# Performance work log

Measured on AMD Instinct MI355X. Metric: run time of the kernel, lower is better.

Reference implementation:

```python
import jax, jax.numpy as jnp
import numpy as np

B, S, D, H, DFF, L = 32, 512, 512, 8, 2048, 3
DK = D // H
NEG = -1e32


def _ln(x, g, b):
    m = jnp.mean(x, axis=-1, keepdims=True)
    v = jnp.mean((x - m) ** 2, axis=-1, keepdims=True)
    return (x - m) / jnp.sqrt(v + 1e-5) * g + b


def _mha(query, key, value, mask, zero_pad, gam, Wk, bk, Wv, bv, Wo, bo):
    # kq_same: q and k both use k_linear
    q = (query @ Wk + bk).reshape(B, S, H, DK).transpose(0, 2, 1, 3)
    k = (key @ Wk + bk).reshape(B, S, H, DK).transpose(0, 2, 1, 3)
    v = (value @ Wv + bv).reshape(B, S, H, DK).transpose(0, 2, 1, 3)
    scores = jnp.einsum('bhid,bhjd->bhij', q, k) / jnp.sqrt(jnp.float32(DK))
    # distance-decay rescoring (no-grad in original)
    p = jax.nn.softmax(jnp.where(mask, scores, NEG), axis=-1) * mask
    distcum = jnp.cumsum(p, axis=-1)
    disttotal = jnp.sum(p, axis=-1, keepdims=True)
    idx = jnp.arange(S)
    pos = jnp.abs(idx[None, :] - idx[:, None]).astype(jnp.float32)  # [S,S]
    dist = jax.lax.stop_gradient(
        jnp.sqrt(jnp.clip((disttotal - distcum) * pos[None, None], 0.0, None)))
    gamma = -jax.nn.softplus(gam)[None, :, None, None]  # [1,H,1,1]
    total_effect = jnp.clip(jnp.exp(dist * gamma), 1e-5, 1e5)
    scores = jnp.where(mask, scores * total_effect, NEG)
    scores = jax.nn.softmax(scores, axis=-1)
    if zero_pad:
        scores = scores * (idx[:, None] > 0)[None, None, :, :].astype(scores.dtype) * 0 + \
                 scores * (idx > 0).astype(scores.dtype)[None, None, :, None]
    out = jnp.einsum('bhij,bhjd->bhid', scores, v)
    out = out.transpose(0, 2, 1, 3).reshape(B, S, D)
    return out @ Wo + bo


def _layer(i, mask, zero_pad, query, key, values, apply_pos,
           Wk, bk, Wv, bv, Wo, bo, gammas, ln1_g, ln1_b, W1, b1, W2, b2, ln2_g, ln2_b):
    a = _mha(query, key, values, mask, zero_pad, gammas[i],
             Wk[i], bk[i], Wv[i], bv[i], Wo[i], bo[i])
    x = _ln(query + a, ln1_g[i], ln1_b[i])
    if apply_pos:
        f = jax.nn.relu(x @ W1[i] + b1[i]) @ W2[i] + b2[i]
        x = _ln(x + f, ln2_g[i], ln2_b[i])
    return x


def setup_inputs() -> dict:
    key = jax.random.key(0)
    ks = jax.random.split(key, 12)
    sc = 0.02
    inp = {
        'q_embed_data': jax.random.normal(ks[0], (B, S, D), jnp.float32),
        'qa_embed_data': jax.random.normal(ks[1], (B, S, D), jnp.float32),
        'Wk': jax.random.normal(ks[2], (L, D, D), jnp.float32) * sc,
        'bk': jnp.zeros((L, D), jnp.float32),
        'Wv': jax.random.normal(ks[3], (L, D, D), jnp.float32) * sc,
        'bv': jnp.zeros((L, D), jnp.float32),
        'Wo': jax.random.normal(ks[4], (L, D, D), jnp.float32) * sc,
        'bo': jnp.zeros((L, D), jnp.float32),
        'gammas': jax.random.normal(ks[5], (L, H), jnp.float32) * 0.5,
        'ln1_g': jnp.ones((L, D), jnp.float32),
        'ln1_b': jnp.zeros((L, D), jnp.float32),
        'W1': jax.random.normal(ks[6], (L, D, DFF), jnp.float32) * sc,
        'b1': jnp.zeros((L, DFF), jnp.float32),
        'W2': jax.random.normal(ks[7], (L, DFF, D), jnp.float32) * sc,
        'b2': jnp.zeros((L, D), jnp.float32),
        'ln2_g': jnp.ones((L, D), jnp.float32),
        'ln2_b': jnp.zeros((L, D), jnp.float32),
    }
    return inp


def reference(q_embed_data, qa_embed_data, Wk, bk, Wv, bv, Wo, bo, gammas,
              ln1_g, ln1_b, W1, b1, W2, b2, ln2_g, ln2_b):
    P = (Wk, bk, Wv, bv, Wo, bo, gammas, ln1_g, ln1_b, W1, b1, W2, b2, ln2_g, ln2_b)
    mask1 = jnp.tril(jnp.ones((S, S), bool), 0)[None, None]   # peek current+past
    mask0 = jnp.tril(jnp.ones((S, S), bool), -1)[None, None]  # peek only past
    y = qa_embed_data
    x = q_embed_data
    # blocks_1 (n_blocks=1): mask=1, self-attn, apply_pos
    y = _layer(0, mask1, False, y, y, y, True, *P)
    # blocks_2 (2 layers): first mask=1 no FFN, second mask=0 zero_pad cross-attn to y
    x = _layer(1, mask1, False, x, x, x, False, *P)
    x = _layer(2, mask0, True, x, x, y, True, *P)
    return x
```

## Files before the change

### kernel.cpp

```cpp
#include <hip/hip_runtime.h>

#define BB   32
#define SS   512
#define DDIM 512
#define HH   8
#define DFFN 2048
#define MR   (BB*SS)

typedef unsigned int   u32;
typedef unsigned short u16;
typedef unsigned char  u8;
typedef __attribute__((ext_vector_type(8))) short bf16x8;
typedef __attribute__((ext_vector_type(4))) float f32x4;

__device__ __forceinline__ u32 packbf2(float x, float y) {
  u32 ux = __float_as_uint(x), uy = __float_as_uint(y);
  u32 hx = (ux + 0x7FFFu + ((ux >> 16) & 1u)) >> 16;
  u32 hy = (uy + 0x7FFFu + ((uy >> 16) & 1u)) >> 16;
  return hx | (hy << 16);
}
__device__ __forceinline__ u16 pack1bf(float x) {
  u32 u = __float_as_uint(x);
  return (u16)((u + 0x7FFFu + ((u >> 16) & 1u)) >> 16);
}

__device__ __forceinline__ float redsum2(float v) {
  v += __shfl_xor(v, 16, 64);
  v += __shfl_xor(v, 32, 64);
  return v;
}

__device__ __forceinline__ float expc(float x) { return __expf(fminf(x, 80.f)); }

__global__ __launch_bounds__(256) void pack_flat(const float* __restrict__ in,
                                                 u16* __restrict__ out) {
  size_t i = ((size_t)blockIdx.x * 256 + threadIdx.x) * 8;
  float4 a = *(const float4*)(in + i);
  float4 b = *(const float4*)(in + i + 4);
  uint4 o;
  o.x = packbf2(a.x, a.y); o.y = packbf2(a.z, a.w);
  o.z = packbf2(b.x, b.y); o.w = packbf2(b.z, b.w);
  *(uint4*)(out + i) = o;
}

__global__ __launch_bounds__(256) void pack_w_t(const float* __restrict__ in,
                                                u16* __restrict__ out, int K, int N) {
  __shared__ float tile[64][65];
  const int t  = threadIdx.x;
  const int n0 = blockIdx.x * 64, k0 = blockIdx.y * 64;
  in  += (size_t)blockIdx.z * K * N;
  out += (size_t)blockIdx.z * N * K;
  #pragma unroll
  for (int it = 0; it < 4; ++it) {
    int idx = it * 256 + t;
    int kk = idx >> 4, n4 = idx & 15;
    float4 v = *(const float4*)(in + (size_t)(k0 + kk) * N + n0 + n4 * 4);
    tile[kk][n4*4+0] = v.x; tile[kk][n4*4+1] = v.y;
    tile[kk][n4*4+2] = v.z; tile[kk][n4*4+3] = v.w;
  }
  __syncthreads();
  #pragma unroll
  for (int it = 0; it < 4; ++it) {
    int idx = it * 256 + t;
    int nn = idx >> 4, g = idx & 15;
    uint2 o;
    o.x = packbf2(tile[g*4+0][nn], tile[g*4+1][nn]);
    o.y = packbf2(tile[g*4+2][nn], tile[g*4+3][nn]);
    *(uint2*)(out + (size_t)(n0 + nn) * K + k0 + g * 4) = o;
  }
}

__global__ __launch_bounds__(512, 2) void gemm8(
    const u16* __restrict__ Aa, const u16* __restrict__ Ab, int lda,
    const u16* __restrict__ Ba, const u16* __restrict__ Bb, int ldb,
    const float* __restrict__ biasa, const float* __restrict__ biasb,
    float* __restrict__ outFa, float* __restrict__ outFb,
    u16* __restrict__ outBa, u16* __restrict__ outBb,
    int ldc, int Kz, int relu, float sca, float scb)
{
  __shared__ __align__(16) u8 lds[131072];

  const int z = blockIdx.z;
  const u16* A    = z ? Ab : Aa;
  const u16* Bt   = z ? Bb : Ba;
  const float* bias = z ? biasb : biasa;
  float* outF = z ? outFb : outFa;
  u16*   outB = z ? outBb : outBa;
  const float sc = z ? scb : sca;

  const int nwg  = gridDim.x * gridDim.y;
  const int orig = blockIdx.y * gridDim.x + blockIdx.x;
  const int q8   = nwg >> 3, r8 = nwg & 7;
  const int xcd  = orig & 7, idx8 = orig >> 3;
  const int wg   = (xcd < r8 ? xcd * (q8 + 1) : r8 * (q8 + 1) + (xcd - r8) * q8) + idx8;
  const int bx   = wg % gridDim.x, by = wg / gridDim.x;
  const int row0 = by * 256, col0 = bx * 256;

  const int t    = threadIdx.x;
  const int lane = t & 63, wid = t >> 6;
  const int wm   = wid >> 2, wn = wid & 3;
  const int rl   = lane & 15, kg = lane >> 4;

  const int NT = Kz >> 6;

  f32x4 acc[8][4] = {};

  auto stageA = [&](int buf, int h, int kt) {
    #pragma unroll
    for (int l = 0; l < 2; ++l) {
      int s  = (l * 512 + t) >> 3;
      int kb = ((lane & 7) * 16) ^ ((s & 7) << 4);
      int row = row0 + ((s >> 6) * 128) + h * 64 + (s & 63);
      const u8* src = (const u8*)A + (size_t)row * lda * 2 + (size_t)kt * 128 + kb;
      u8* dst = lds + buf * 65536 + h * 16384 + (l * 512 + wid * 64) * 16;
      __builtin_amdgcn_global_load_lds(
          (const __attribute__((address_space(1))) u32*)src,
          (__attribute__((address_space(3))) u32*)dst, 16, 0, 0);
    }
  };
  auto stageB = [&](int buf, int h, int kt) {
    #pragma unroll
    for (int l = 0; l < 2; ++l) {
      int s  = (l * 512 + t) >> 3;
      int kb = ((lane & 7) * 16) ^ ((s & 7) << 4);
      int col = col0 + ((s >> 5) * 64) + h * 32 + (s & 31);
      const u8* src = (const u8*)Bt + (size_t)col * ldb * 2 + (size_t)kt * 128 + kb;
      u8* dst = lds + buf * 65536 + 32768 + h * 16384 + (l * 512 + wid * 64) * 16;
      __builtin_amdgcn_global_load_lds(
          (const __attribute__((address_space(1))) u32*)src,
          (__attribute__((address_space(3))) u32*)dst, 16, 0, 0);
    }
  };

  auto rdA = [&](int buf, int mh, int m, int ks) -> bf16x8 {
    int s = wm * 64 + m * 16 + rl;
    int off = buf * 65536 + mh * 16384 + s * 128 + (((ks * 32 + kg * 8) * 2) ^ ((s & 7) << 4));
    return *(const bf16x8*)(lds + off);
  };
  auto rdB = [&](int buf, int nh, int n, int ks) -> bf16x8 {
    int s = wn * 32 + n * 16 + rl;
    int off = buf * 65536 + 32768 + nh * 16384 + s * 128 + (((ks * 32 + kg * 8) * 2) ^ ((s & 7) << 4));
    return *(const bf16x8*)(lds + off);
  };

#define GBAR asm volatile("s_barrier" ::: "memory")
#define VMW4 asm volatile("s_waitcnt vmcnt(4)" ::: "memory")

#define PHASE(BUF, MH, NH, STAGECODE, DOVM) do {                               \
    bf16x8 af_[4][2], bf_[2][2];                                               \
    _Pragma("unroll") for (int m_ = 0; m_ < 4; ++m_)                           \
      _Pragma("unroll") for (int k_ = 0; k_ < 2; ++k_)                         \
        af_[m_][k_] = rdA(BUF, MH, m_, k_);                                    \
    _Pragma("unroll") for (int n_ = 0; n_ < 2; ++n_)                           \
      _Pragma("unroll") for (int k_ = 0; k_ < 2; ++k_)                         \
        bf_[n_][k_] = rdB(BUF, NH, n_, k_);                                    \
    STAGECODE;                                                                 \
    if (DOVM) VMW4;                                                            \
    GBAR;                                                                      \
    __builtin_amdgcn_s_setprio(1);                                             \
    _Pragma("unroll") for (int m_ = 0; m_ < 4; ++m_)                           \
      _Pragma("unroll") for (int n_ = 0; n_ < 2; ++n_) {                       \
        acc[(MH)*4+m_][(NH)*2+n_] = __builtin_amdgcn_mfma_f32_16x16x32_bf16(   \
            af_[m_][0], bf_[n_][0], acc[(MH)*4+m_][(NH)*2+n_], 0, 0, 0);       \
        acc[(MH)*4+m_][(NH)*2+n_] = __builtin_amdgcn_mfma_f32_16x16x32_bf16(   \
            af_[m_][1], bf_[n_][1], acc[(MH)*4+m_][(NH)*2+n_], 0, 0, 0);       \
      }                                                                        \
    __builtin_amdgcn_s_setprio(0);                                             \
    GBAR;                                                                      \
  } while (0)

  stageA(0, 0, 0); stageB(0, 0, 0); stageA(0, 1, 0); stageB(0, 1, 0);
  stageA(1, 0, 1); stageB(1, 0, 1);
  VMW4; GBAR;

  for (int i = 0; i < (NT >> 1); ++i) {
    const int T1 = 2 * i + 1;
    int T2 = 2 * i + 2; if (T2 >= NT) T2 -= NT;
    int T3 = 2 * i + 3; if (T3 >= NT) T3 -= NT;
    PHASE(0, 0, 0, stageA(1, 1, T1), 0);
    PHASE(0, 0, 1, stageB(1, 1, T1), 0);
    PHASE(0, 1, 0, stageA(0, 0, T2), 0);
    PHASE(0, 1, 1, stageB(0, 0, T2), 1);
    PHASE(1, 0, 0, stageA(0, 1, T2), 0);
    PHASE(1, 0, 1, stageB(0, 1, T2), 0);
    PHASE(1, 1, 0, stageA(1, 0, T3), 0);
    PHASE(1, 1, 1, stageB(1, 0, T3), 1);
  }
#undef PHASE
#undef GBAR
#undef VMW4

  #pragma unroll
  for (int M = 0; M < 8; ++M) {
    #pragma unroll
    for (int N2 = 0; N2 < 4; ++N2) {
      const int col = col0 + wn * 64 + N2 * 16 + rl;
      const float bs = bias ? bias[col] : 0.f;
      #pragma unroll
      for (int q = 0; q < 4; ++q) {
        const int row = row0 + wm * 128 + M * 16 + kg * 4 + q;
        float v = (acc[M][N2][q] + bs) * sc;
        if (relu) v = fmaxf(v, 0.f);
        if (outF) outF[(size_t)row * ldc + col] = v;
        if (outB) outB[(size_t)row * ldc + col] = pack1bf(v);
      }
    }
  }
}

__global__ __attribute__((amdgpu_flat_work_group_size(512, 512)))
           __attribute__((amdgpu_waves_per_eu(1, 2)))
void attn_mfma(
    const u16* __restrict__ qk, const u16* __restrict__ vbuf,
    const float* __restrict__ gam, u16* __restrict__ out,
    int mask_excl, int zero_pad)
{
  __shared__ __align__(16) u8 kSb[65536];
  __shared__ __align__(16) u8 vTb[65536];
  __shared__ __align__(16) u8 pChb[8192];

  const int t    = threadIdx.x;
  const int lane = t & 63, wid = t >> 6;
  const int ql   = lane & 15, g = lane >> 4;
  const int bh   = blockIdx.x, b = bh >> 3, h = bh & 7;
  const size_t base = (size_t)b * SS * DDIM + (size_t)h * 64;

  float gv = gam[h];
  float sp = (gv > 0.f) ? (gv + log1pf(__expf(-gv))) : log1pf(__expf(gv));
  const float gamma = -sp;

  for (int it = 0; it < 8; ++it) {
    int idx = it * 512 + t;
    int j = idx >> 3, u = idx & 7;
    uint4 w = *(const uint4*)(qk + base + (size_t)j * DDIM + u * 8);
    *(uint4*)(kSb + ((j * 128 + u * 16) ^ ((j & 7) << 4))) = w;
  }
  for (int it = 0; it < 8; ++it) {
    int idx = it * 512 + t;
    int j = idx >> 3, u = idx & 7;
    union { uint4 v4; u16 s[8]; } uu;
    uu.v4 = *(const uint4*)(vbuf + base + (size_t)j * DDIM + u * 8);
    #pragma unroll
    for (int dd = 0; dd < 8; ++dd) {
      int d = u * 8 + dd;
      *(u16*)(vTb + d * 1024 + ((2 * j) ^ ((dd ^ u) << 4))) = uu.s[dd];
    }
  }
  __syncthreads();

  bool vm[4];
  #pragma unroll
  for (int rg = 0; rg < 4; ++rg) {
    int kl = 4 * g + rg;
    vm[rg] = mask_excl ? (kl < ql) : (kl <= ql);
  }

  u8* pB = pChb + wid * 1024;
  const int swp = (ql & 7) << 4;

  int vbase[4], vsw[4];
  #pragma unroll
  for (int n = 0; n < 4; ++n) {
    int d = n * 16 + ql;
    vbase[n] = d * 1024;
    vsw[n]   = ((d & 7) ^ ((d >> 3) & 7)) << 4;
  }

  #pragma unroll
  for (int ri = 0; ri < 4; ++ri) {
    int r0_ = (ri == 0) ? wid : (ri == 1) ? (15 - wid) : (ri == 2) ? (16 + wid) : (31 - wid);
    const int rs = __builtin_amdgcn_readfirstlane(r0_);
    const int i0 = rs * 16;

    const int qrow = i0 + ql;
    const int qsw  = (qrow & 7) << 4;
    bf16x8 qf0 = *(const bf16x8*)(kSb + ((qrow * 128      + g * 16) ^ qsw));
    bf16x8 qf1 = *(const bf16x8*)(kSb + ((qrow * 128 + 64 + g * 16) ^ qsw));

    float S1l = 0.f;
    #pragma unroll
    for (int kt = 0; kt < 32; ++kt) {
      if (kt <= rs) {
        const bool dg = (kt == rs);
        const int krow = kt * 16 + ql;
        const int ksw  = (krow & 7) << 4;
        bf16x8 ka0 = *(const bf16x8*)(kSb + ((krow * 128      + g * 16) ^ ksw));
        bf16x8 ka1 = *(const bf16x8*)(kSb + ((krow * 128 + 64 + g * 16) ^ ksw));
        f32x4 dv = {};
        dv = __builtin_amdgcn_mfma_f32_16x16x32_bf16(ka0, qf0, dv, 0, 0, 0);
        dv = __builtin_amdgcn_mfma_f32_16x16x32_bf16(ka1, qf1, dv, 0, 0, 0);
        float e0 = (!dg || vm[0]) ? expc(dv[0]) : 0.f;
        float e1 = (!dg || vm[1]) ? expc(dv[1]) : 0.f;
        float e2 = (!dg || vm[2]) ? expc(dv[2]) : 0.f;
        float e3 = (!dg || vm[3]) ? expc(dv[3]) : 0.f;
        S1l += (e0 + e1) + (e2 + e3);
      }
    }
    const float S1   = redsum2(S1l);
    const float inv1 = (S1 > 0.f) ? (1.f / S1) : 0.f;

    f32x4 oacc[4] = {};
    float cbase = 0.f, S2l = 0.f;
    const float qlf = (float)(i0 + ql);

    auto subkt = [&](int kt, bool dg, u32& wA, u32& wB) {
      const int krow = kt * 16 + ql;
      const int ksw  = (krow & 7) << 4;
      bf16x8 ka0 = *(const bf16x8*)(kSb + ((krow * 128      + g * 16) ^ ksw));
      bf16x8 ka1 = *(const bf16x8*)(kSb + ((krow * 128 + 64 + g * 16) ^ ksw));
      f32x4 dv = {};
      dv = __builtin_amdgcn_mfma_f32_16x16x32_bf16(ka0, qf0, dv, 0, 0, 0);
      dv = __builtin_amdgcn_mfma_f32_16x16x32_bf16(ka1, qf1, dv, 0, 0, 0);
      const bool v0 = !dg || vm[0], v1 = !dg || vm[1];
      const bool v2 = !dg || vm[2], v3 = !dg || vm[3];
      float e0 = v0 ? expc(dv[0]) : 0.f;
      float e1 = v1 ? expc(dv[1]) : 0.f;
      float e2 = v2 ? expc(dv[2]) : 0.f;
      float e3 = v3 ? expc(dv[3]) : 0.f;
      float p0 = e0, p1 = p0 + e1, p2 = p1 + e2, p3 = p2 + e3;
      float a16 = __shfl_up(p3, 16, 64);
      float a32 = __shfl_up(p3, 32, 64);
      float a48 = __shfl_up(p3, 48, 64);
      float gp = (g >= 1 ? a16 : 0.f) + (g >= 2 ? a32 : 0.f) + (g >= 3 ? a48 : 0.f);
      float tt = __shfl(gp + p3, ql + 48, 64);
      const float pbase = cbase + gp;
      const float pf = qlf - (float)(kt * 16 + 4 * g);
      float ipr[4] = {p0, p1, p2, p3};
      bool  vv[4]  = {v0, v1, v2, v3};
      float sv[4]  = {dv[0], dv[1], dv[2], dv[3]};
      float q2[4];
      #pragma unroll
      for (int rg = 0; rg < 4; ++rg) {
        float rem  = fmaxf((S1 - (pbase + ipr[rg])) * inv1, 0.f);
        float pos  = pf - (float)rg;
        float dist = sqrtf(fmaxf(rem * pos, 0.f));
        float eff  = fmaxf(__expf(gamma * dist), 1e-5f);
        float ee   = vv[rg] ? expc(sv[rg] * eff) : 0.f;
        q2[rg] = ee;
        S2l += ee;
      }
      wA = packbf2(q2[0], q2[1]);
      wB = packbf2(q2[2], q2[3]);
      cbase += tt;
    };

    #pragma unroll
    for (int c = 0; c < 16; ++c) {
      if (2 * c <= rs) {
        u32 w0 = 0, w1 = 0, w2 = 0, w3 = 0;
        subkt(2 * c, (2 * c == rs), w0, w1);
        if (2 * c + 1 <= rs) subkt(2 * c + 1, (2 * c + 1 == rs), w2, w3);
        *(u32*)(pB + ((ql * 64 +      8 * g    ) ^ swp)) = w0;
        *(u32*)(pB + ((ql * 64 +      8 * g + 4) ^ swp)) = w1;
        *(u32*)(pB + ((ql * 64 + 32 + 8 * g    ) ^ swp)) = w2;
        *(u32*)(pB + ((ql * 64 + 32 + 8 * g + 4) ^ swp)) = w3;
        bf16x8 pa = *(const bf16x8*)(pB + ((ql * 64 + 16 * g) ^ swp));
        #pragma unroll
        for (int n = 0; n < 4; ++n) {
          bf16x8 vb = *(const bf16x8*)(vTb + vbase[n] + ((64 * c + 16 * g) ^ vsw[n]));
          oacc[n] = __builtin_amdgcn_mfma_f32_16x16x32_bf16(pa, vb, oacc[n], 0, 0, 0);
        }
      }
    }

    const float S2   = redsum2(S2l);
    const float inv2 = 1.f / fmaxf(S2, 1e-30f);
    float i2[4];
    #pragma unroll
    for (int rg = 0; rg < 4; ++rg) i2[rg] = __shfl(inv2, 4 * g + rg, 64);

    #pragma unroll
    for (int n = 0; n < 4; ++n) {
      #pragma unroll
      for (int rg = 0; rg < 4; ++rg) {
        const int qo = i0 + 4 * g + rg;
        float val = oacc[n][rg] * i2[rg];
        if (zero_pad && qo == 0) val = 0.f;
        out[base + (size_t)qo * DDIM + n * 16 + ql] = pack1bf(val);
      }
    }
  }
}

__global__ __launch_bounds__(256) void ln_kernel(
    const u16* __restrict__ a, const float* __restrict__ bsrc,
    const float* __restrict__ csrc,
    const float* __restrict__ g, const float* __restrict__ be,
    float* __restrict__ outF, u16* __restrict__ outB)
{
  const int lane = threadIdx.x & 63, w = threadIdx.x >> 6;
  const size_t row = (size_t)blockIdx.x * 4 + w;
  const size_t off8 = row * DDIM + lane * 8;

  uint4 ab = *(const uint4*)(a + off8);
  const u16* ap = (const u16*)&ab;
  float v[8];
  #pragma unroll
  for (int k = 0; k < 8; ++k) v[k] = __uint_as_float(((u32)ap[k]) << 16);

  float4 b0 = *(const float4*)(bsrc + off8);
  float4 b1 = *(const float4*)(bsrc + off8 + 4);
  v[0] += b0.x; v[1] += b0.y; v[2] += b0.z; v[3] += b0.w;
  v[4] += b1.x; v[5] += b1.y; v[6] += b1.z; v[7] += b1.w;
  if (csrc) {
    float4 c0 = *(const float4*)(csrc + off8);
    float4 c1 = *(const float4*)(csrc + off8 + 4);
    v[0] += c0.x; v[1] += c0.y; v[2] += c0.z; v[3] += c0.w;
    v[4] += c1.x; v[5] += c1.y; v[6] += c1.z; v[7] += c1.w;
  }

  float sum = 0.f;
  #pragma unroll
  for (int k = 0; k < 8; ++k) sum += v[k];
  #pragma unroll
  for (int off = 32; off > 0; off >>= 1) sum += __shfl_xor(sum, off, 64);
  const float mean = sum * (1.f / 512.f);
  float var = 0.f;
  #pragma unroll
  for (int k = 0; k < 8; ++k) { float dd = v[k] - mean; var = fmaf(dd, dd, var); }
  #pragma unroll
  for (int off = 32; off > 0; off >>= 1) var += __shfl_xor(var, off, 64);
  var *= (1.f / 512.f);
  const float inv = rsqrtf(var + 1e-5f);

  float4 g0 = *(const float4*)(g + lane * 8);
  float4 g1 = *(const float4*)(g + lane * 8 + 4);
  float4 e0 = *(const float4*)(be + lane * 8);
  float4 e1 = *(const float4*)(be + lane * 8 + 4);
  float gv[8] = {g0.x, g0.y, g0.z, g0.w, g1.x, g1.y, g1.z, g1.w};
  float ev[8] = {e0.x, e0.y, e0.z, e0.w, e1.x, e1.y, e1.z, e1.w};
  float o[8];
  #pragma unroll
  for (int k = 0; k < 8; ++k) o[k] = (v[k] - mean) * inv * gv[k] + ev[k];

  if (outF) {
    float4 f0 = {o[0], o[1], o[2], o[3]};
    float4 f1 = {o[4], o[5], o[6], o[7]};
    *(float4*)(outF + off8)     = f0;
    *(float4*)(outF + off8 + 4) = f1;
  }
  if (outB) {
    uint4 p;
    p.x = packbf2(o[0], o[1]); p.y = packbf2(o[2], o[3]);
    p.z = packbf2(o[4], o[5]); p.w = packbf2(o[6], o[7]);
    *(uint4*)(outB + off8) = p;
  }
}

extern "C" void kernel_launch(void* const* d_in, const int* in_sizes, int n_in,
                              void* d_out, int out_size, void* d_ws, size_t ws_size,
                              hipStream_t stream) {
  const float* qe  = (const float*)d_in[0];
  const float* qa  = (const float*)d_in[1];
  const float* Wk  = (const float*)d_in[2];
  const float* bk  = (const float*)d_in[3];
  const float* Wv  = (const float*)d_in[4];
  const float* bv  = (const float*)d_in[5];
  const float* Wo  = (const float*)d_in[6];
  const float* bo  = (const float*)d_in[7];
  const float* gm  = (const float*)d_in[8];
  const float* l1g = (const float*)d_in[9];
  const float* l1b = (const float*)d_in[10];
  const float* W1  = (const float*)d_in[11];
  const float* b1  = (const float*)d_in[12];
  const float* W2  = (const float*)d_in[13];
  const float* b2  = (const float*)d_in[14];
  const float* l2g = (const float*)d_in[15];
  const float* l2b = (const float*)d_in[16];

  char* ws = (char*)d_ws;
  u16* WT = (u16*)ws;
  u16* A0 = (u16*)(ws + ((size_t)18  << 20));
  u16* A1 = (u16*)(ws + ((size_t)34  << 20));
  u16* A2 = (u16*)(ws + ((size_t)50  << 20));
  u16* A3 = (u16*)(ws + ((size_t)66  << 20));
  float* F0 = (float*)(ws + ((size_t)82  << 20));
  float* PW2 = (float*)(ws + ((size_t)114 << 20));
  u16* Amid = (u16*)(ws + ((size_t)146 << 20));
  float* PWo = (float*)Amid;

  u16* WkT = WT;
  u16* WvT = WT + (size_t)3 * 262144;
  u16* WoT = WT + (size_t)6 * 262144;
  u16* W1T = WT + (size_t)9 * 262144;
  u16* W2T = W1T + (size_t)3 * 1048576;

  pack_w_t<<<dim3(8, 8, 3),  256, 0, stream>>>(Wk, WkT, 512, 512);
  pack_w_t<<<dim3(8, 8, 3),  256, 0, stream>>>(Wv, WvT, 512, 512);
  pack_w_t<<<dim3(8, 8, 3),  256, 0, stream>>>(Wo, WoT, 512, 512);
  pack_w_t<<<dim3(32, 8, 3), 256, 0, stream>>>(W1, W1T, 512, 2048);
  pack_w_t<<<dim3(8, 32, 3), 256, 0, stream>>>(W2, W2T, 2048, 512);
  pack_flat<<<4096, 256, 0, stream>>>(qa, A0);
  pack_flat<<<4096, 256, 0, stream>>>(qe, A1);

  const float SQ = 0.35355339059327373f;

  auto g8 = [&](const u16* Aa, const u16* Ab, int lda,
                const u16* Ba, const u16* Bb, int ldb,
                const float* ba, const float* bb,
                float* oFa, float* oFb, u16* oBa, u16* oBb,
                int ldc, int M, int N, int Kz, int relu, int nz,
                float sca, float scb) {
    gemm8<<<dim3(N / 256, M / 256, nz), 512, 0, stream>>>(
        Aa, Ab, lda, Ba, Bb, ldb, ba, bb, oFa, oFb, oBa, oBb, ldc, Kz, relu,
        sca, scb);
  };

  auto layer = [&](int li, const u16* qbf, const u16* vbf,
                   int excl, int zp, int pos,
                   u16* x1B, u16* y2B, float* y2F) {
    const float* bk_l = bk + (size_t)li * DDIM;
    const float* bv_l = bv + (size_t)li * DDIM;
    const float* bo_l = bo + (size_t)li * DDIM;
    const float* gm_l = gm + (size_t)li * HH;
    const float* g1   = l1g + (size_t)li * DDIM;
    const float* be1  = l1b + (size_t)li * DDIM;
    const float* g2   = l2g + (size_t)li * DDIM;
    const float* be2  = l2b + (size_t)li * DDIM;
    const float* b1_l = b1 + (size_t)li * DFFN;
    const float* b2_l = b2 + (size_t)li * DDIM;
    const u16* WkT_l = WkT + (size_t)li * 262144;
    const u16* WvT_l = WvT + (size_t)li * 262144;
    const u16* WoT_l = WoT + (size_t)li * 262144;
    const u16* W1T_l = W1T + (size_t)li * 1048576;
    const u16* W2T_l = W2T + (size_t)li * 1048576;

    g8(qbf, vbf, 512, WkT_l, WvT_l, 512, bk_l, bv_l,
       nullptr, nullptr, A2, A3, 512, MR, 512, 512, 0, 2, SQ, 1.f);
    attn_mfma<<<BB * HH, 512, 0, stream>>>(A2, A3, gm_l, A3, excl, zp);
    g8(A3, A3 + 256, 512, WoT_l, WoT_l + 256, 512, bo_l, nullptr,
       F0, PWo, nullptr, nullptr, 512, MR, 512, 256, 0, 2, 1.f, 1.f);
    ln_kernel<<<MR / 4, 256, 0, stream>>>(qbf, F0, PWo, g1, be1, nullptr, x1B);
    if (pos) {
      g8(x1B, nullptr, 512, W1T_l, nullptr, 512, b1_l, nullptr,
         nullptr, nullptr, Amid, nullptr, 2048, MR, 2048, 512, 1, 1, 1.f, 1.f);
      g8(Amid, Amid + 1024, 2048, W2T_l, W2T_l + 1024, 2048, b2_l, nullptr,
         F0, PW2, nullptr, nullptr, 512, MR, 512, 1024, 0, 2, 1.f, 1.f);
      ln_kernel<<<MR / 4, 256, 0, stream>>>(x1B, F0, PW2, g2, be2, y2F, y2B);
    }
  };

  layer(0, A0, A0, 0, 0, 1, A2, A0, nullptr);
  layer(1, A1, A1, 0, 0, 0, A1, nullptr, nullptr);
  layer(2, A1, A0, 1, 1, 1, A1, nullptr, (float*)d_out);
}
```

Baseline: 700.0 us.

## Batch independent layer-0/1 attention stages into shared launches and use exp2

Layers 0 and 1 are independent up to their first LayerNorm, so their QKV projections, attention, output projections and LayerNorms now run together in single launches via job tables (4-way and 2-way grid z), raising occupancy for the smaller grids. Attention switches to base-2 exponentials with the log2e factor folded into the QK scale and gamma. The V transpose now writes packed 32-bit pairs. The GEMM loop gets a peeled tail that skips the wrap-around prefetch. Weight and input packing kernels are merged to cut launches, at the cost of more workspace buffers and a larger kernel parameter struct.

Result: faster. 656.5 us (-6.2%).

```diff
diff --git a/kernel.cpp b/kernel.cpp
--- a/kernel.cpp
+++ b/kernel.cpp
@@ -30,10 +30,27 @@
   return v;
 }
 
-__device__ __forceinline__ float expc(float x) { return __expf(fminf(x, 80.f)); }
-
-__global__ __launch_bounds__(256) void pack_flat(const float* __restrict__ in,
-                                                 u16* __restrict__ out) {
+#if __has_builtin(__builtin_amdgcn_exp2f)
+__device__ __forceinline__ float ex2c(float x) { return __builtin_amdgcn_exp2f(fminf(x, 110.f)); }
+__device__ __forceinline__ float ex2r(float x) { return __builtin_amdgcn_exp2f(x); }
+#else
+__device__ __forceinline__ float ex2c(float x) {
+  float r = fminf(x, 110.f);
+  asm("v_exp_f32 %0, %1" : "=v"(r) : "v"(r));
+  return r;
+}
+__device__ __forceinline__ float ex2r(float x) {
+  float r;
+  asm("v_exp_f32 %0, %1" : "=v"(r) : "v"(x));
+  return r;
+}
+#endif
+
+__global__ __launch_bounds__(256) void pack_flat2(
+    const float* __restrict__ in0, const float* __restrict__ in1,
+    u16* __restrict__ out0, u16* __restrict__ out1) {
+  const float* in = blockIdx.y ? in1 : in0;
+  u16* out = blockIdx.y ? out1 : out0;
   size_t i = ((size_t)blockIdx.x * 256 + threadIdx.x) * 8;
   float4 a = *(const float4*)(in + i);
   float4 b = *(const float4*)(in + i + 4);
@@ -43,13 +60,12 @@
   *(uint4*)(out + i) = o;
 }
 
-__global__ __launch_bounds__(256) void pack_w_t(const float* __restrict__ in,
-                                                u16* __restrict__ out, int K, int N) {
+__device__ __forceinline__ void wtp_body(const float* __restrict__ in,
+                                         u16* __restrict__ out, int K, int N,
+                                         int bx, int by) {
   __shared__ float tile[64][65];
   const int t  = threadIdx.x;
-  const int n0 = blockIdx.x * 64, k0 = blockIdx.y * 64;
-  in  += (size_t)blockIdx.z * K * N;
-  out += (size_t)blockIdx.z * N * K;
+  const int n0 = bx * 64, k0 = by * 64;
   #pragma unroll
   for (int it = 0; it < 4; ++it) {
     int idx = it * 256 + t;
@@ -69,24 +85,37 @@
     *(uint2*)(out + (size_t)(n0 + nn) * K + k0 + g * 4) = o;
   }
 }
+__global__ __launch_bounds__(256) void pack_w_t(const float* __restrict__ in,
+                                                u16* __restrict__ out, int K, int N) {
+  wtp_body(in + (size_t)blockIdx.z * K * N, out + (size_t)blockIdx.z * N * K,
+           K, N, blockIdx.x, blockIdx.y);
+}
+__global__ __launch_bounds__(256) void pack_w_sq(
+    const float* __restrict__ Wk, const float* __restrict__ Wv,
+    const float* __restrict__ Wo,
+    u16* __restrict__ WkT, u16* __restrict__ WvT, u16* __restrict__ WoT) {
+  const int z = blockIdx.z, which = z / 3, li = z % 3;
+  const float* in = (which == 0 ? Wk : which == 1 ? Wv : Wo) + (size_t)li * 262144;
+  u16* out = (which == 0 ? WkT : which == 1 ? WvT : WoT) + (size_t)li * 262144;
+  wtp_body(in, out, 512, 512, blockIdx.x, blockIdx.y);
+}
+
+struct GJob { const u16* A; const u16* Bt; const float* bias;
+              float* outF; u16* outB; float sc; };
+struct GJobs { GJob j[4]; };
 
 __global__ __launch_bounds__(512, 2) void gemm8(
-    const u16* __restrict__ Aa, const u16* __restrict__ Ab, int lda,
-    const u16* __restrict__ Ba, const u16* __restrict__ Bb, int ldb,
-    const float* __restrict__ biasa, const float* __restrict__ biasb,
-    float* __restrict__ outFa, float* __restrict__ outFb,
-    u16* __restrict__ outBa, u16* __restrict__ outBb,
-    int ldc, int Kz, int relu, float sca, float scb)
+    GJobs jobs, int lda, int ldb, int ldc, int Kz, int relu)
 {
   __shared__ __align__(16) u8 lds[131072];
 
-  const int z = blockIdx.z;
-  const u16* A    = z ? Ab : Aa;
-  const u16* Bt   = z ? Bb : Ba;
-  const float* bias = z ? biasb : biasa;
-  float* outF = z ? outFb : outFa;
-  u16*   outB = z ? outBb : outBa;
-  const float sc = z ? scb : sca;
+  const GJob J = jobs.j[blockIdx.z];
+  const u16* A    = J.A;
+  const u16* Bt   = J.Bt;
+  const float* bias = J.bias;
+  float* outF = J.outF;
+  u16*   outB = J.outB;
+  const float sc = J.sc;
 
   const int nwg  = gridDim.x * gridDim.y;
   const int orig = blockIdx.y * gridDim.x + blockIdx.x;
@@ -145,6 +174,7 @@
 
 #define GBAR asm volatile("s_barrier" ::: "memory")
 #define VMW4 asm volatile("s_waitcnt vmcnt(4)" ::: "memory")
+#define VMW0 asm volatile("s_waitcnt vmcnt(0)" ::: "memory")
 
 #define PHASE(BUF, MH, NH, STAGECODE, DOVM) do {                               \
     bf16x8 af_[4][2], bf_[2][2];                                               \
@@ -155,7 +185,8 @@
       _Pragma("unroll") for (int k_ = 0; k_ < 2; ++k_)                         \
         bf_[n_][k_] = rdB(BUF, NH, n_, k_);                                    \
     STAGECODE;                                                                 \
-    if (DOVM) VMW4;                                                            \
+    if (DOVM == 1) VMW4;                                                       \
+    if (DOVM == 2) VMW0;                                                       \
     GBAR;                                                                      \
     __builtin_amdgcn_s_setprio(1);                                             \
     _Pragma("unroll") for (int m_ = 0; m_ < 4; ++m_)                           \
@@ -173,10 +204,8 @@
   stageA(1, 0, 1); stageB(1, 0, 1);
   VMW4; GBAR;
 
-  for (int i = 0; i < (NT >> 1); ++i) {
-    const int T1 = 2 * i + 1;
-    int T2 = 2 * i + 2; if (T2 >= NT) T2 -= NT;
-    int T3 = 2 * i + 3; if (T3 >= NT) T3 -= NT;
+  for (int i = 0; i < (NT >> 1) - 1; ++i) {
+    const int T1 = 2 * i + 1, T2 = 2 * i + 2, T3 = 2 * i + 3;
     PHASE(0, 0, 0, stageA(1, 1, T1), 0);
     PHASE(0, 0, 1, stageB(1, 1, T1), 0);
     PHASE(0, 1, 0, stageA(0, 0, T2), 0);
@@ -186,9 +215,18 @@
     PHASE(1, 1, 0, stageA(1, 0, T3), 0);
     PHASE(1, 1, 1, stageB(1, 0, T3), 1);
   }
+  PHASE(0, 0, 0, stageA(1, 1, NT - 1), 0);
+  PHASE(0, 0, 1, stageB(1, 1, NT - 1), 0);
+  PHASE(0, 1, 0, ;, 0);
+  PHASE(0, 1, 1, ;, 2);
+  PHASE(1, 0, 0, ;, 0);
+  PHASE(1, 0, 1, ;, 0);
+  PHASE(1, 1, 0, ;, 0);
+  PHASE(1, 1, 1, ;, 0);
 #undef PHASE
 #undef GBAR
 #undef VMW4
+#undef VMW0
 
   #pragma unroll
   for (int M = 0; M < 8; ++M) {
@@ -211,9 +249,11 @@
 __global__ __attribute__((amdgpu_flat_work_group_size(512, 512)))
            __attribute__((amdgpu_waves_per_eu(1, 2)))
 void attn_mfma(
-    const u16* __restrict__ qk, const u16* __restrict__ vbuf,
-    const float* __restrict__ gam, u16* __restrict__ out,
-    int mask_excl, int zero_pad)
+    const u16* __restrict__ qkA, const u16* __restrict__ vbA,
+    const float* __restrict__ gmA, u16* __restrict__ outAp,
+    const u16* __restrict__ qkB, const u16* __restrict__ vbB,
+    const float* __restrict__ gmB, u16* __restrict__ outBp,
+    int nA, int mask_excl, int zero_pad)
 {
   __shared__ __align__(16) u8 kSb[65536];
   __shared__ __align__(16) u8 vTb[65536];
@@ -222,12 +262,19 @@
   const int t    = threadIdx.x;
   const int lane = t & 63, wid = t >> 6;
   const int ql   = lane & 15, g = lane >> 4;
-  const int bh   = blockIdx.x, b = bh >> 3, h = bh & 7;
+  const int bid  = blockIdx.x;
+  const int sel  = bid >= nA;
+  const u16* qk    = sel ? qkB : qkA;
+  const u16* vbuf  = sel ? vbB : vbA;
+  const float* gam = sel ? gmB : gmA;
+  u16* out         = sel ? outBp : outAp;
+  const int bh = sel ? bid - nA : bid;
+  const int b = bh >> 3, h = bh & 7;
   const size_t base = (size_t)b * SS * DDIM + (size_t)h * 64;
 
   float gv = gam[h];
   float sp = (gv > 0.f) ? (gv + log1pf(__expf(-gv))) : log1pf(__expf(gv));
-  const float gamma = -sp;
+  const float gamma2 = -sp * 1.442695041f;
 
   for (int it = 0; it < 8; ++it) {
     int idx = it * 512 + t;
@@ -235,15 +282,19 @@
     uint4 w = *(const uint4*)(qk + base + (size_t)j * DDIM + u * 8);
     *(uint4*)(kSb + ((j * 128 + u * 16) ^ ((j & 7) << 4))) = w;
   }
-  for (int it = 0; it < 8; ++it) {
+  for (int it = 0; it < 4; ++it) {
     int idx = it * 512 + t;
-    int j = idx >> 3, u = idx & 7;
-    union { uint4 v4; u16 s[8]; } uu;
-    uu.v4 = *(const uint4*)(vbuf + base + (size_t)j * DDIM + u * 8);
+    int jp = idx >> 3, u = idx & 7;
+    const u16* src = vbuf + base + (size_t)(2 * jp) * DDIM + u * 8;
+    uint4 r0 = *(const uint4*)src;
+    uint4 r1 = *(const uint4*)(src + DDIM);
+    const u16* a0 = (const u16*)&r0;
+    const u16* a1 = (const u16*)&r1;
     #pragma unroll
     for (int dd = 0; dd < 8; ++dd) {
       int d = u * 8 + dd;
-      *(u16*)(vTb + d * 1024 + ((2 * j) ^ ((dd ^ u) << 4))) = uu.s[dd];
+      u32 w = (u32)a0[dd] | ((u32)a1[dd] << 16);
+      *(u32*)(vTb + d * 1024 + ((4 * jp) ^ ((dd ^ u) << 4))) = w;
     }
   }
   __syncthreads();
@@ -289,10 +340,10 @@
         f32x4 dv = {};
         dv = __builtin_amdgcn_mfma_f32_16x16x32_bf16(ka0, qf0, dv, 0, 0, 0);
         dv = __builtin_amdgcn_mfma_f32_16x16x32_bf16(ka1, qf1, dv, 0, 0, 0);
-        float e0 = (!dg || vm[0]) ? expc(dv[0]) : 0.f;
-        float e1 = (!dg || vm[1]) ? expc(dv[1]) : 0.f;
-        float e2 = (!dg || vm[2]) ? expc(dv[2]) : 0.f;
-        float e3 = (!dg || vm[3]) ? expc(dv[3]) : 0.f;
+        float e0 = (!dg || vm[0]) ? ex2c(dv[0]) : 0.f;
+        float e1 = (!dg || vm[1]) ? ex2c(dv[1]) : 0.f;
+        float e2 = (!dg || vm[2]) ? ex2c(dv[2]) : 0.f;
+        float e3 = (!dg || vm[3]) ? ex2c(dv[3]) : 0.f;
         S1l += (e0 + e1) + (e2 + e3);
       }
     }
@@ -313,10 +364,10 @@
       dv = __builtin_amdgcn_mfma_f32_16x16x32_bf16(ka1, qf1, dv, 0, 0, 0);
       const bool v0 = !dg || vm[0], v1 = !dg || vm[1];
       const bool v2 = !dg || vm[2], v3 = !dg || vm[3];
-      float e0 = v0 ? expc(dv[0]) : 0.f;
-      float e1 = v1 ? expc(dv[1]) : 0.f;
-      float e2 = v2 ? expc(dv[2]) : 0.f;
-      float e3 = v3 ? expc(dv[3]) : 0.f;
+      float e0 = v0 ? ex2c(dv[0]) : 0.f;
+      float e1 = v1 ? ex2c(dv[1]) : 0.f;
+      float e2 = v2 ? ex2c(dv[2]) : 0.f;
+      float e3 = v3 ? ex2c(dv[3]) : 0.f;
       float p0 = e0, p1 = p0 + e1, p2 = p1 + e2, p3 = p2 + e3;
       float a16 = __shfl_up(p3, 16, 64);
       float a32 = __shfl_up(p3, 32, 64);
@@ -334,8 +385,8 @@
         float rem  = fmaxf((S1 - (pbase + ipr[rg])) * inv1, 0.f);
         float pos  = pf - (float)rg;
         float dist = sqrtf(fmaxf(rem * pos, 0.f));
-        float eff  = fmaxf(__expf(gamma * dist), 1e-5f);
-        float ee   = vv[rg] ? expc(sv[rg] * eff) : 0.f;
+        float eff  = fmaxf(ex2r(gamma2 * dist), 1e-5f);
+        float ee   = vv[rg] ? ex2c(sv[rg] * eff) : 0.f;
         q2[rg] = ee;
         S2l += ee;
       }
@@ -382,29 +433,30 @@
   }
 }
 
-__global__ __launch_bounds__(256) void ln_kernel(
-    const u16* __restrict__ a, const float* __restrict__ bsrc,
-    const float* __restrict__ csrc,
-    const float* __restrict__ g, const float* __restrict__ be,
-    float* __restrict__ outF, u16* __restrict__ outB)
+struct LNJob { const u16* a; const float* b; const float* c;
+               const float* g; const float* be; float* outF; u16* outB; };
+struct LNJobs { LNJob j[2]; };
+
+__global__ __launch_bounds__(256) void ln_kernel(LNJobs jobs)
 {
+  const LNJob J = jobs.j[blockIdx.y];
   const int lane = threadIdx.x & 63, w = threadIdx.x >> 6;
   const size_t row = (size_t)blockIdx.x * 4 + w;
   const size_t off8 = row * DDIM + lane * 8;
 
-  uint4 ab = *(const uint4*)(a + off8);
+  uint4 ab = *(const uint4*)(J.a + off8);
   const u16* ap = (const u16*)&ab;
   float v[8];
   #pragma unroll
   for (int k = 0; k < 8; ++k) v[k] = __uint_as_float(((u32)ap[k]) << 16);
 
-  float4 b0 = *(const float4*)(bsrc + off8);
-  float4 b1 = *(const float4*)(bsrc + off8 + 4);
+  float4 b0 = *(const float4*)(J.b + off8);
+  float4 b1 = *(const float4*)(J.b + off8 + 4);
   v[0] += b0.x; v[1] += b0.y; v[2] += b0.z; v[3] += b0.w;
   v[4] += b1.x; v[5] += b1.y; v[6] += b1.z; v[7] += b1.w;
-  if (csrc) {
-    float4 c0 = *(const float4*)(csrc + off8);
-    float4 c1 = *(const float4*)(csrc + off8 + 4);
+  if (J.c) {
+    float4 c0 = *(const float4*)(J.c + off8);
+    float4 c1 = *(const float4*)(J.c + off8 + 4);
     v[0] += c0.x; v[1] += c0.y; v[2] += c0.z; v[3] += c0.w;
     v[4] += c1.x; v[5] += c1.y; v[6] += c1.z; v[7] += c1.w;
   }
@@ -423,27 +475,27 @@
   var *= (1.f / 512.f);
   const float inv = rsqrtf(var + 1e-5f);
 
-  float4 g0 = *(const float4*)(g + lane * 8);
-  float4 g1 = *(const float4*)(g + lane * 8 + 4);
-  float4 e0 = *(const float4*)(be + lane * 8);
-  float4 e1 = *(const float4*)(be + lane * 8 + 4);
+  float4 g0 = *(const float4*)(J.g + lane * 8);
+  float4 g1 = *(const float4*)(J.g + lane * 8 + 4);
+  float4 e0 = *(const float4*)(J.be + lane * 8);
+  float4 e1 = *(const float4*)(J.be + lane * 8 + 4);
   float gv[8] = {g0.x, g0.y, g0.z, g0.w, g1.x, g1.y, g1.z, g1.w};
   float ev[8] = {e0.x, e0.y, e0.z, e0.w, e1.x, e1.y, e1.z, e1.w};
   float o[8];
   #pragma unroll
   for (int k = 0; k < 8; ++k) o[k] = (v[k] - mean) * inv * gv[k] + ev[k];
 
-  if (outF) {
+  if (J.outF) {
     float4 f0 = {o[0], o[1], o[2], o[3]};
     float4 f1 = {o[4], o[5], o[6], o[7]};
-    *(float4*)(outF + off8)     = f0;
-    *(float4*)(outF + off8 + 4) = f1;
-  }
-  if (outB) {
+    *(float4*)(J.outF + off8)     = f0;
+    *(float4*)(J.outF + off8 + 4) = f1;
+  }
+  if (J.outB) {
     uint4 p;
     p.x = packbf2(o[0], o[1]); p.y = packbf2(o[2], o[3]);
     p.z = packbf2(o[4], o[5]); p.w = packbf2(o[6], o[7]);
-    *(uint4*)(outB + off8) = p;
+    *(uint4*)(J.outB + off8) = p;
   }
 }
 
@@ -469,15 +521,17 @@
   const float* l2b = (const float*)d_in[16];
 
   char* ws = (char*)d_ws;
-  u16* WT = (u16*)ws;
-  u16* A0 = (u16*)(ws + ((size_t)18  << 20));
-  u16* A1 = (u16*)(ws + ((size_t)34  << 20));
-  u16* A2 = (u16*)(ws + ((size_t)50  << 20));
-  u16* A3 = (u16*)(ws + ((size_t)66  << 20));
-  float* F0 = (float*)(ws + ((size_t)82  << 20));
-  float* PW2 = (float*)(ws + ((size_t)114 << 20));
-  u16* Amid = (u16*)(ws + ((size_t)146 << 20));
-  float* PWo = (float*)Amid;
+  u16* WT  = (u16*)ws;
+  u16* A0  = (u16*)(ws + ((size_t)18  << 20));
+  u16* A1  = (u16*)(ws + ((size_t)34  << 20));
+  u16* A2  = (u16*)(ws + ((size_t)50  << 20));
+  u16* A3  = (u16*)(ws + ((size_t)66  << 20));
+  u16* A4  = (u16*)(ws + ((size_t)82  << 20));
+  u16* A5  = (u16*)(ws + ((size_t)98  << 20));
+  float* F0a = (float*)(ws + ((size_t)114 << 20));
+  u16* X0  = (u16*)(ws + ((size_t)146 << 20));
+  float* G1  = (float*)(ws + ((size_t)162 << 20));
+  u16* Amid = A2;
 
   u16* WkT = WT;
   u16* WvT = WT + (size_t)3 * 262144;
@@ -485,62 +539,82 @@
   u16* W1T = WT + (size_t)9 * 262144;
   u16* W2T = W1T + (size_t)3 * 1048576;
 
-  pack_w_t<<<dim3(8, 8, 3),  256, 0, stream>>>(Wk, WkT, 512, 512);
-  pack_w_t<<<dim3(8, 8, 3),  256, 0, stream>>>(Wv, WvT, 512, 512);
-  pack_w_t<<<dim3(8, 8, 3),  256, 0, stream>>>(Wo, WoT, 512, 512);
+  pack_w_sq<<<dim3(8, 8, 9),  256, 0, stream>>>(Wk, Wv, Wo, WkT, WvT, WoT);
   pack_w_t<<<dim3(32, 8, 3), 256, 0, stream>>>(W1, W1T, 512, 2048);
   pack_w_t<<<dim3(8, 32, 3), 256, 0, stream>>>(W2, W2T, 2048, 512);
-  pack_flat<<<4096, 256, 0, stream>>>(qa, A0);
-  pack_flat<<<4096, 256, 0, stream>>>(qe, A1);
-
-  const float SQ = 0.35355339059327373f;
-
-  auto g8 = [&](const u16* Aa, const u16* Ab, int lda,
-                const u16* Ba, const u16* Bb, int ldb,
-                const float* ba, const float* bb,
-                float* oFa, float* oFb, u16* oBa, u16* oBb,
-                int ldc, int M, int N, int Kz, int relu, int nz,
-                float sca, float scb) {
+  pack_flat2<<<dim3(4096, 2), 256, 0, stream>>>(qa, qe, A0, A1);
+
+  const float SQ2 = 0.4246609001f;
+
+  auto g8 = [&](GJobs jobs, int lda, int ldb, int ldc,
+                int M, int N, int Kz, int relu, int nz) {
     gemm8<<<dim3(N / 256, M / 256, nz), 512, 0, stream>>>(
-        Aa, Ab, lda, Ba, Bb, ldb, ba, bb, oFa, oFb, oBa, oBb, ldc, Kz, relu,
-        sca, scb);
+        jobs, lda, ldb, ldc, Kz, relu);
   };
-
-  auto layer = [&](int li, const u16* qbf, const u16* vbf,
-                   int excl, int zp, int pos,
-                   u16* x1B, u16* y2B, float* y2F) {
-    const float* bk_l = bk + (size_t)li * DDIM;
-    const float* bv_l = bv + (size_t)li * DDIM;
-    const float* bo_l = bo + (size_t)li * DDIM;
-    const float* gm_l = gm + (size_t)li * HH;
-    const float* g1   = l1g + (size_t)li * DDIM;
-    const float* be1  = l1b + (size_t)li * DDIM;
-    const float* g2   = l2g + (size_t)li * DDIM;
-    const float* be2  = l2b + (size_t)li * DDIM;
-    const float* b1_l = b1 + (size_t)li * DFFN;
-    const float* b2_l = b2 + (size_t)li * DDIM;
-    const u16* WkT_l = WkT + (size_t)li * 262144;
-    const u16* WvT_l = WvT + (size_t)li * 262144;
-    const u16* WoT_l = WoT + (size_t)li * 262144;
-    const u16* W1T_l = W1T + (size_t)li * 1048576;
-    const u16* W2T_l = W2T + (size_t)li * 1048576;
-
-    g8(qbf, vbf, 512, WkT_l, WvT_l, 512, bk_l, bv_l,
-       nullptr, nullptr, A2, A3, 512, MR, 512, 512, 0, 2, SQ, 1.f);
-    attn_mfma<<<BB * HH, 512, 0, stream>>>(A2, A3, gm_l, A3, excl, zp);
-    g8(A3, A3 + 256, 512, WoT_l, WoT_l + 256, 512, bo_l, nullptr,
-       F0, PWo, nullptr, nullptr, 512, MR, 512, 256, 0, 2, 1.f, 1.f);
-    ln_kernel<<<MR / 4, 256, 0, stream>>>(qbf, F0, PWo, g1, be1, nullptr, x1B);
-    if (pos) {
-      g8(x1B, nullptr, 512, W1T_l, nullptr, 512, b1_l, nullptr,
-         nullptr, nullptr, Amid, nullptr, 2048, MR, 2048, 512, 1, 1, 1.f, 1.f);
-      g8(Amid, Amid + 1024, 2048, W2T_l, W2T_l + 1024, 2048, b2_l, nullptr,
-         F0, PW2, nullptr, nullptr, 512, MR, 512, 1024, 0, 2, 1.f, 1.f);
-      ln_kernel<<<MR / 4, 256, 0, stream>>>(x1B, F0, PW2, g2, be2, y2F, y2B);
-    }
+  auto ln2x = [&](LNJobs jobs, int nz) {
+    ln_kernel<<<dim3(MR / 4, nz), 256, 0, stream>>>(jobs);
   };
 
-  layer(0, A0, A0, 0, 0, 1, A2, A0, nullptr);
-  layer(1, A1, A1, 0, 0, 0, A1, nullptr, nullptr);
-  layer(2, A1, A0, 1, 1, 1, A1, nullptr, (float*)d_out);
-}
+  auto WkT_l = [&](int l){ return WkT + (size_t)l * 262144; };
+  auto WvT_l = [&](int l){ return WvT + (size_t)l * 262144; };
+  auto WoT_l = [&](int l){ return WoT + (size_t)l * 262144; };
+  auto W1T_l = [&](int l){ return W1T + (size_t)l * 1048576; };
+  auto W2T_l = [&](int l){ return W2T + (size_t)l * 1048576; };
+
+  {
+    GJobs pj = {{ {A0, WkT_l(0), bk,       nullptr, A2, SQ2},
+                  {A0, WvT_l(0), bv,       nullptr, A3, 1.f},
+                  {A1, WkT_l(1), bk + 512, nullptr, A4, SQ2},
+                  {A1, WvT_l(1), bv + 512, nullptr, A5, 1.f} }};
+    g8(pj, 512, 512, 512, MR, 512, 512, 0, 4);
+
+    attn_mfma<<<BB * HH * 2, 512, 0, stream>>>(
+        A2, A3, gm, A3, A4, A5, gm + HH, A5, BB * HH, 0, 0);
+
+    GJobs wj = {{ {A3, WoT_l(0), bo,       F0a, nullptr, 1.f},
+                  {A5, WoT_l(1), bo + 512, G1,  nullptr, 1.f},
+                  {}, {} }};
+    g8(wj, 512, 512, 512, MR, 512, 512, 0, 2);
+
+    LNJobs lj = {{ {A0, F0a, nullptr, l1g,       l1b,       nullptr, X0},
+                   {A1, G1,  nullptr, l1g + 512, l1b + 512, nullptr, A1} }};
+    ln2x(lj, 2);
+  }
+  {
+    GJobs w1j = {{ {X0, W1T_l(0), b1, nullptr, Amid, 1.f}, {}, {}, {} }};
+    g8(w1j, 512, 512, 2048, MR, 2048, 512, 1, 1);
+    GJobs w2j = {{ {Amid,        W2T_l(0),        b2,      F0a, nullptr, 1.f},
+                   {Amid + 1024, W2T_l(0) + 1024, nullptr, G1,  nullptr, 1.f},
+                   {}, {} }};
+    g8(w2j, 2048, 2048, 512, MR, 512, 1024, 0, 2);
+    LNJobs lj = {{ {X0, F0a, G1, l2g, l2b, nullptr, A0}, {} }};
+    ln2x(lj, 1);
+  }
+  {
+    GJobs pj = {{ {A1, WkT_l(2), bk + 1024, nullptr, A2, SQ2},
+                  {A0, WvT_l(2), bv + 1024, nullptr, A3, 1.f},
+                  {}, {} }};
+    g8(pj, 512, 512, 512, MR, 512, 512, 0, 2);
+
+    attn_mfma<<<BB * HH, 512, 0, stream>>>(
+        A2, A3, gm + 2 * HH, A3, A2, A3, gm + 2 * HH, A3, BB * HH, 1, 1);
+
+    GJobs wj = {{ {A3,       WoT_l(2),       bo + 1024, F0a, nullptr, 1.f},
+                  {A3 + 256, WoT_l(2) + 256, nullptr,   G1,  nullptr, 1.f},
+                  {}, {} }};
+    g8(wj, 512, 512, 512, MR, 512, 256, 0, 2);
+
+    LNJobs l1j = {{ {A1, F0a, G1, l1g + 1024, l1b + 1024, nullptr, A1}, {} }};
+    ln2x(l1j, 1);
+
+    GJobs w1j = {{ {A1, W1T_l(2), b1 + 2 * DFFN, nullptr, Amid, 1.f}, {}, {}, {} }};
+    g8(w1j, 512, 512, 2048, MR, 2048, 512, 1, 1);
+    GJobs w2j = {{ {Amid,        W2T_l(2),        b2 + 1024, F0a, nullptr, 1.f},
+                   {Amid + 1024, W2T_l(2) + 1024, nullptr,   G1,  nullptr, 1.f},
+                   {}, {} }};
+    g8(w2j, 2048, 2048, 512, MR, 512, 1024, 0, 2);
+
+    LNJobs l2j = {{ {A1, F0a, G1, l2g + 1024, l2b + 1024, (float*)d_out, nullptr}, {} }};
+    ln2x(l2j, 1);
+  }
+}
```
